# Optimization experiments

Hardware: AMD Instinct MI355X
Metric: run time of the kernel (lower is better)

The kernel has to match this reference:

```python
import jax, jax.numpy as jnp
import numpy as np

D = 2  # spatial dimension


def _conv_contract(image, filt, in_k, out_k):
    """Tensor convolution + contraction on a torus.
    image: (in_c, N, N) + (D,)*in_k
    filt:  (out_c, in_c, M, M) + (D,)*in_k + (D,)*out_k
    out:   (out_c, N, N) + (D,)*out_k
    Image tensor indices contract with the first in_k filter tensor indices.
    """
    in_c, N = image.shape[0], image.shape[1]
    out_c, M = filt.shape[0], filt.shape[2]
    di, do = D ** in_k, D ** out_k
    # fold tensor indices into channels: (1, in_c*di, N, N)
    img = jnp.transpose(image.reshape(in_c, N, N, di), (0, 3, 1, 2)).reshape(1, in_c * di, N, N)
    # filter -> (out_c*do, in_c*di, M, M), ordering (out_c, out_idx, in_c, in_idx)
    f = filt.reshape(out_c, in_c, M, M, di, do)
    f = jnp.transpose(f, (0, 5, 1, 4, 2, 3)).reshape(out_c * do, in_c * di, M, M)
    p = M // 2
    img = jnp.pad(img, ((0, 0), (0, 0), (p, p), (p, p)), mode='wrap')  # torus
    out = jax.lax.conv_general_dilated(
        img, f, window_strides=(1, 1), padding='VALID',
        dimension_numbers=('NCHW', 'OIHW', 'NCHW'))[0]
    out = jnp.transpose(out.reshape(out_c, do, N, N), (0, 2, 3, 1))
    return out.reshape((out_c, N, N) + (D,) * out_k)


def _synth(w, fils):
    # (out_c, in_c, n) x (n, M, M, tensor...) -> (out_c, in_c, M, M, tensor...)
    return jnp.einsum('oik,k...->oi...', w, fils)


def setup_inputs() -> dict:
    key = jax.random.key(0)
    ks = jax.random.split(key, 11)
    r = lambda k, s: jax.random.normal(k, s, dtype=jnp.float32)
    return {
        'x0': r(ks[0], (64, 256, 256)),
        'x1': r(ks[1], (64, 256, 256, 2)),
        'fil0': r(ks[2], (3, 3, 3)),
        'fil1': r(ks[3], (6, 3, 3, 2)),
        'fil2': r(ks[4], (12, 3, 3, 2, 2)),
        'w00': r(ks[5], (64, 64, 3)) * (1.0 / np.sqrt(64 * 3)),
        'w01': r(ks[6], (64, 64, 6)) * (1.0 / np.sqrt(64 * 6)),
        'w10': r(ks[7], (64, 64, 6)) * (1.0 / np.sqrt(64 * 6)),
        'w11': r(ks[8], (64, 64, 12)) * (1.0 / np.sqrt(64 * 12)),
        'b0': r(ks[9], (64, 1, 1)) * 0.05,
        'b1': r(ks[10], (64, 1, 1, 1)) * 0.05,
    }


def reference(x0, x1, fil0, fil1, fil2, w00, w01, w10, w11, b0, b1):
    # accumulate over input blocks for each target (out_k, out_p=0)
    out0 = _conv_contract(x0, _synth(w00, fil0), 0, 0) \
         + _conv_contract(x1, _synth(w10, fil1), 1, 0)
    out1 = _conv_contract(x0, _synth(w01, fil1), 0, 1) \
         + _conv_contract(x1, _synth(w11, fil2), 1, 1)
    # use_bias='auto': plain bias for scalars, mean-scaled bias for tensors
    out0 = out0 + b0
    mean1 = jnp.mean(out1, axis=(1, 2), keepdims=True)  # spatial mean
    out1 = out1 + mean1 * b1
    return (out0, out1)
```

## Files before the change

kernel.cpp:

```cpp
#include <hip/hip_runtime.h>
#include <hip/hip_bf16.h>
#include <string.h>


#define NN 256
#define NPIX 65536
#define OUT1_OFF 4194304

typedef __attribute__((ext_vector_type(8))) short short8;
typedef __attribute__((ext_vector_type(4))) float floatx4;

__device__ __forceinline__ unsigned short f2b(float x) {
    unsigned int u; memcpy(&u, &x, 4);
    return (unsigned short)((u + 0x7FFFu + ((u >> 16) & 1u)) >> 16);
}

__global__ __launch_bounds__(256) void prep_kernel(const float* __restrict__ x0,
                                                   const float* __restrict__ x1,
                                                   unsigned short* __restrict__ Xb) {
    const int x = threadIdx.x;
    const int y = blockIdx.x;
    const int c = blockIdx.y;
    unsigned int u[8];
    if (c < 4) {
        const float* base = x0 + ((size_t)c * 16) * NPIX + y * NN + x;
#pragma unroll
        for (int j = 0; j < 8; j++) {
            unsigned short a = f2b(base[(size_t)(2 * j) * NPIX]);
            unsigned short b = f2b(base[(size_t)(2 * j + 1) * NPIX]);
            u[j] = (unsigned int)a | ((unsigned int)b << 16);
        }
    } else {
        const float2* base = (const float2*)x1 + ((size_t)(8 * (c - 4))) * NPIX + y * NN + x;
#pragma unroll
        for (int j = 0; j < 8; j++) {
            float2 v = base[(size_t)j * NPIX];
            u[j] = (unsigned int)f2b(v.x) | ((unsigned int)f2b(v.y) << 16);
        }
    }
    uint4* dst = (uint4*)(Xb + (((size_t)y * 12 + c) * 256 + x) * 16);
    dst[0] = make_uint4(u[0], u[1], u[2], u[3]);
    dst[1] = make_uint4(u[4], u[5], u[6], u[7]);
}

__global__ void synth_kernel(const float* __restrict__ fil0, const float* __restrict__ fil1,
                             const float* __restrict__ fil2,
                             const float* __restrict__ w00, const float* __restrict__ w01,
                             const float* __restrict__ w10, const float* __restrict__ w11,
                             unsigned short* __restrict__ Fb) {
    int idx = blockIdx.x * 256 + threadIdx.x;
    if (idx >= 12 * 192 * 160) return;
    int kpos = idx % 160;
    int co   = (idx / 160) % 192;
    int c    = idx / (160 * 192);
    int tap = kpos >> 4, cl = kpos & 15;
    float s = 0.0f;
    if (tap < 9) {
        int cin = c * 16 + cl;
        if (co < 64) {
            if (cin < 64) {
                for (int k = 0; k < 3; k++)
                    s += w00[(co * 64 + cin) * 3 + k] * fil0[k * 9 + tap];
            } else {
                int i = (cin - 64) >> 1, t = (cin - 64) & 1;
                for (int k = 0; k < 6; k++)
                    s += w10[(co * 64 + i) * 6 + k] * fil1[(k * 9 + tap) * 2 + t];
            }
        } else {
            int o = (co - 64) >> 1, u = (co - 64) & 1;
            if (cin < 64) {
                for (int k = 0; k < 6; k++)
                    s += w01[(o * 64 + cin) * 6 + k] * fil1[(k * 9 + tap) * 2 + u];
            } else {
                int i = (cin - 64) >> 1, t = (cin - 64) & 1;
                for (int k = 0; k < 12; k++)
                    s += w11[(o * 64 + i) * 12 + k] * fil2[((k * 9 + tap) * 2 + t) * 2 + u];
            }
        }
    }
    Fb[idx] = f2b(s);
}

__global__ __launch_bounds__(512, 4) void conv_kernel(
    const unsigned short* __restrict__ Xb, const unsigned short* __restrict__ Fb,
    const float* __restrict__ b0, float* __restrict__ out,
    float* __restrict__ mean_partial) {

    __shared__ __align__(16) unsigned short Flds[96 * 160];
    __shared__ __align__(16) unsigned short Xlds[3 * 256 * 16];
    __shared__ float red[96][4];

    const int tid = threadIdx.x;
    const int y = blockIdx.x;
    const int m0 = blockIdx.y * 96;
    const int l = tid & 63, w = tid >> 6;
    const int wm = w >> 2, wn = w & 3;
    const int mw = wm * 48, nw = wn * 64;
    const int ln = l & 15, quad = l >> 4;

    int baseA[3];
#pragma unroll
    for (int f = 0; f < 3; f++) baseA[f] = (mw + f * 16 + ln) * 160 + quad * 8;
    int cb[4];
#pragma unroll
    for (int g = 0; g < 4; g++) cb[g] = nw + g * 16 + ln;
    int rofs[5], dxv[5];
#pragma unroll
    for (int ks = 0; ks < 5; ks++) {
        int tap = 2 * ks + (quad >> 1);
        int r, dx;
        if (tap > 8) { r = 0; dx = 0; }
        else { r = tap / 3; dx = tap - 3 * r - 1; }
        rofs[ks] = r * 4096 + (quad & 1) * 8;
        dxv[ks] = dx;
    }

    floatx4 acc[3][4];
#pragma unroll
    for (int f = 0; f < 3; f++)
#pragma unroll
        for (int g = 0; g < 4; g++) acc[f][g] = (floatx4){0.f, 0.f, 0.f, 0.f};

    for (int c = 0; c < 12; c++) {
        const unsigned short* FbC = Fb + ((size_t)c * 192 + m0) * 160;
        for (int s = w; s < 54; s += 8) {
            const unsigned short* g;
            unsigned short* lb;
            if (s < 30) {
                g = FbC + s * 512;
                lb = Flds + s * 512;
            } else {
                int j = s - 30;
                int r = j >> 3, p = j & 7;
                int yr = (y + r + 255) & 255;
                g = Xb + (((size_t)yr * 12 + c) * 4096) + p * 512;
                lb = Xlds + r * 4096 + p * 512;
            }
            __builtin_amdgcn_global_load_lds(
                (const __attribute__((address_space(1))) unsigned int*)(g + l * 8),
                (__attribute__((address_space(3))) unsigned int*)lb, 16, 0, 0);
        }
        __syncthreads();

#pragma unroll
        for (int ks = 0; ks < 5; ks++) {
            short8 A[3], B[4];
#pragma unroll
            for (int f = 0; f < 3; f++)
                A[f] = *(const short8*)(Flds + baseA[f] + ks * 32);
#pragma unroll
            for (int g = 0; g < 4; g++) {
                int colw = (cb[g] + dxv[ks]) & 255;
                B[g] = *(const short8*)(Xlds + rofs[ks] + colw * 16);
            }
#pragma unroll
            for (int f = 0; f < 3; f++)
#pragma unroll
                for (int g = 0; g < 4; g++)
                    acc[f][g] = __builtin_amdgcn_mfma_f32_16x16x32_bf16(A[f], B[g], acc[f][g], 0, 0, 0);
        }
        __syncthreads();
    }

#pragma unroll
    for (int f = 0; f < 3; f++)
#pragma unroll
        for (int reg = 0; reg < 4; reg++) {
            float s = acc[f][0][reg] + acc[f][1][reg] + acc[f][2][reg] + acc[f][3][reg];
#pragma unroll
            for (int d = 1; d < 16; d <<= 1) s += __shfl_xor(s, d, 64);
            if (ln == 0) red[mw + f * 16 + quad * 4 + reg][wn] = s;
        }

#pragma unroll
    for (int f = 0; f < 3; f++) {
        int cob = m0 + mw + f * 16 + quad * 4;
#pragma unroll
        for (int g = 0; g < 4; g++) {
            int col = nw + g * 16 + ln;
            if (cob < 64) {
#pragma unroll
                for (int reg = 0; reg < 4; reg++)
                    out[(size_t)(cob + reg) * NPIX + y * NN + col] = acc[f][g][reg] + b0[cob + reg];
            } else {
#pragma unroll
                for (int reg = 0; reg < 4; reg += 2) {
                    int o = (cob + reg - 64) >> 1;
                    float2 v = make_float2(acc[f][g][reg], acc[f][g][reg + 1]);
                    *((float2*)(out + OUT1_OFF) + ((size_t)o * NPIX + y * NN + col)) = v;
                }
            }
        }
    }
    __syncthreads();
    if (tid < 96) {
        int co = m0 + tid;
        if (co >= 64) {
            float s = red[tid][0] + red[tid][1] + red[tid][2] + red[tid][3];
            mean_partial[y * 128 + (co - 64)] = s;
        }
    }
}

__global__ void reduce_kernel(const float* __restrict__ mean_partial,
                              const float* __restrict__ b1, float* __restrict__ meanb) {
    int o = blockIdx.x;
    int t = threadIdx.x;
    float s0 = mean_partial[t * 128 + 2 * o];
    float s1 = mean_partial[t * 128 + 2 * o + 1];
#pragma unroll
    for (int d = 1; d < 64; d <<= 1) {
        s0 += __shfl_xor(s0, d, 64);
        s1 += __shfl_xor(s1, d, 64);
    }
    __shared__ float sh[2][4];
    if ((t & 63) == 0) { sh[0][t >> 6] = s0; sh[1][t >> 6] = s1; }
    __syncthreads();
    if (t == 0) {
        float S0 = sh[0][0] + sh[0][1] + sh[0][2] + sh[0][3];
        float S1 = sh[1][0] + sh[1][1] + sh[1][2] + sh[1][3];
        float scale = b1[o] * (1.0f / 65536.0f);
        meanb[2 * o] = S0 * scale;
        meanb[2 * o + 1] = S1 * scale;
    }
}

__global__ void apply_kernel(float* __restrict__ out, const float* __restrict__ meanb) {
    int idx = blockIdx.x * 256 + threadIdx.x;
    int o = idx >> 16;
    float2* p = (float2*)(out + OUT1_OFF) + idx;
    float2 v = *p;
    v.x += meanb[2 * o];
    v.y += meanb[2 * o + 1];
    *p = v;
}

extern "C" void kernel_launch(void* const* d_in, const int* in_sizes, int n_in,
                              void* d_out, int out_size, void* d_ws, size_t ws_size,
                              hipStream_t stream) {
    const float* x0   = (const float*)d_in[0];
    const float* x1   = (const float*)d_in[1];
    const float* fil0 = (const float*)d_in[2];
    const float* fil1 = (const float*)d_in[3];
    const float* fil2 = (const float*)d_in[4];
    const float* w00  = (const float*)d_in[5];
    const float* w01  = (const float*)d_in[6];
    const float* w10  = (const float*)d_in[7];
    const float* w11  = (const float*)d_in[8];
    const float* b0   = (const float*)d_in[9];
    const float* b1   = (const float*)d_in[10];

    unsigned short* Xb  = (unsigned short*)d_ws;
    unsigned short* Fb  = (unsigned short*)((char*)d_ws + 25165824);
    float* mean_partial = (float*)((char*)d_ws + 25903104);
    float* meanb        = (float*)((char*)d_ws + 26034176);
    float* out = (float*)d_out;

    prep_kernel<<<dim3(NN, 12), 256, 0, stream>>>(x0, x1, Xb);

    synth_kernel<<<(12 * 192 * 160 + 255) / 256, 256, 0, stream>>>(
        fil0, fil1, fil2, w00, w01, w10, w11, Fb);

    conv_kernel<<<dim3(NN, 2), 512, 0, stream>>>(Xb, Fb, b0, out, mean_partial);

    reduce_kernel<<<64, 256, 0, stream>>>(mean_partial, b1, meanb);

    apply_kernel<<<NPIX * 64 / 256, 256, 0, stream>>>(out, meanb);
}
```

Before: 175.1 us.

## Compute tensor-output spatial mean from input means and fold into conv epilogue

Uses linearity of the torus convolution to get the spatial mean of out1 from per-channel input means and the filter taps. Input sums are gathered during the bf16 prep pass, which now reads vectorised float4s. This removes the separate reduce and apply passes that re-read and re-wrote the whole out1 tensor, and lets conv add the mean bias directly when it stores. The filter row stride is padded to 168, and the mean is now taken over bf16-rounded filters against fp32 inputs, which slightly changes numerics.

```diff
diff --git a/kernel.cpp b/kernel.cpp
--- a/kernel.cpp
+++ b/kernel.cpp
@@ -6,6 +6,7 @@
 #define NN 256
 #define NPIX 65536
 #define OUT1_OFF 4194304
+#define FS 168
 
 typedef __attribute__((ext_vector_type(8))) short short8;
 typedef __attribute__((ext_vector_type(4))) float floatx4;
@@ -14,33 +15,63 @@
     unsigned int u; memcpy(&u, &x, 4);
     return (unsigned short)((u + 0x7FFFu + ((u >> 16) & 1u)) >> 16);
 }
+__device__ __forceinline__ float b2f16(unsigned short u) {
+    unsigned int v = ((unsigned int)u) << 16; float f; memcpy(&f, &v, 4); return f;
+}
+__device__ __forceinline__ unsigned int pack2(float a, float b) {
+    return (unsigned int)f2b(a) | ((unsigned int)f2b(b) << 16);
+}
 
 __global__ __launch_bounds__(256) void prep_kernel(const float* __restrict__ x0,
                                                    const float* __restrict__ x1,
-                                                   unsigned short* __restrict__ Xb) {
-    const int x = threadIdx.x;
-    const int y = blockIdx.x;
+                                                   unsigned short* __restrict__ Xb,
+                                                   float* __restrict__ partial) {
+    const int t = threadIdx.x;
+    const int w = t >> 6, tx = t & 63;
+    const int y = blockIdx.x * 4 + w;
     const int c = blockIdx.y;
-    unsigned int u[8];
+    const int col0 = tx * 4;
+
+    unsigned int u[4][8];
+    float sum[16];
     if (c < 4) {
-        const float* base = x0 + ((size_t)c * 16) * NPIX + y * NN + x;
-#pragma unroll
+        #pragma unroll
         for (int j = 0; j < 8; j++) {
-            unsigned short a = f2b(base[(size_t)(2 * j) * NPIX]);
-            unsigned short b = f2b(base[(size_t)(2 * j + 1) * NPIX]);
-            u[j] = (unsigned int)a | ((unsigned int)b << 16);
+            const float4 a = *(const float4*)(x0 + (size_t)(16 * c + 2 * j) * NPIX + y * NN + col0);
+            const float4 b = *(const float4*)(x0 + (size_t)(16 * c + 2 * j + 1) * NPIX + y * NN + col0);
+            u[0][j] = pack2(a.x, b.x);
+            u[1][j] = pack2(a.y, b.y);
+            u[2][j] = pack2(a.z, b.z);
+            u[3][j] = pack2(a.w, b.w);
+            sum[2 * j]     = a.x + a.y + a.z + a.w;
+            sum[2 * j + 1] = b.x + b.y + b.z + b.w;
         }
     } else {
-        const float2* base = (const float2*)x1 + ((size_t)(8 * (c - 4))) * NPIX + y * NN + x;
-#pragma unroll
+        #pragma unroll
         for (int j = 0; j < 8; j++) {
-            float2 v = base[(size_t)j * NPIX];
-            u[j] = (unsigned int)f2b(v.x) | ((unsigned int)f2b(v.y) << 16);
-        }
-    }
-    uint4* dst = (uint4*)(Xb + (((size_t)y * 12 + c) * 256 + x) * 16);
-    dst[0] = make_uint4(u[0], u[1], u[2], u[3]);
-    dst[1] = make_uint4(u[4], u[5], u[6], u[7]);
+            int i = 8 * (c - 4) + j;
+            const float* base = x1 + ((size_t)(i * 256 + y) * 256 + col0) * 2;
+            const float4 p0 = *(const float4*)(base);
+            const float4 p1 = *(const float4*)(base + 4);
+            u[0][j] = pack2(p0.x, p0.y);
+            u[1][j] = pack2(p0.z, p0.w);
+            u[2][j] = pack2(p1.x, p1.y);
+            u[3][j] = pack2(p1.z, p1.w);
+            sum[2 * j]     = p0.x + p0.z + p1.x + p1.z;
+            sum[2 * j + 1] = p0.y + p0.w + p1.y + p1.w;
+        }
+    }
+    uint4* dst = (uint4*)(Xb + (((size_t)y * 12 + c) * 256 + col0) * 16);
+    #pragma unroll
+    for (int cc = 0; cc < 4; cc++) {
+        dst[cc * 2]     = make_uint4(u[cc][0], u[cc][1], u[cc][2], u[cc][3]);
+        dst[cc * 2 + 1] = make_uint4(u[cc][4], u[cc][5], u[cc][6], u[cc][7]);
+    }
+    #pragma unroll
+    for (int cl = 0; cl < 16; cl++)
+        #pragma unroll
+        for (int d = 1; d < 64; d <<= 1) sum[cl] += __shfl_xor(sum[cl], d, 64);
+    if (tx < 16) partial[(c * 16 + tx) * 256 + y] = sum[tx];
 }
 
 __global__ void synth_kernel(const float* __restrict__ fil0, const float* __restrict__ fil1,
@@ -49,10 +80,10 @@
                              const float* __restrict__ w10, const float* __restrict__ w11,
                              unsigned short* __restrict__ Fb) {
     int idx = blockIdx.x * 256 + threadIdx.x;
-    if (idx >= 12 * 192 * 160) return;
-    int kpos = idx % 160;
-    int co   = (idx / 160) % 192;
-    int c    = idx / (160 * 192);
+    if (idx >= 12 * 192 * FS) return;
+    int kpos = idx % FS;
+    int co   = (idx / FS) % 192;
+    int c    = idx / (FS * 192);
     int tap = kpos >> 4, cl = kpos & 15;
     float s = 0.0f;
     if (tap < 9) {
@@ -81,14 +112,40 @@
     Fb[idx] = f2b(s);
 }
 
+__global__ void meanx_kernel(const float* __restrict__ partial, float* __restrict__ meanX) {
+    int cin = blockIdx.x * 64 + threadIdx.x;
+    const float4* p = (const float4*)(partial + (size_t)cin * 256);
+    float s = 0.0f;
+    for (int j = 0; j < 64; j++) { float4 v = p[j]; s += v.x + v.y + v.z + v.w; }
+    meanX[cin] = s * (1.0f / 65536.0f);
+}
+
+__global__ void meanb_kernel(const unsigned short* __restrict__ Fb,
+                             const float* __restrict__ meanX,
+                             const float* __restrict__ b1, float* __restrict__ meanb) {
+    int c1 = blockIdx.x;
+    int l = threadIdx.x;
+    int co = 64 + c1;
+    float s = 0.0f;
+    for (int c = 0; c < 12; c++) {
+        const unsigned short* row = Fb + ((size_t)c * 192 + co) * FS;
+        for (int idx = l; idx < 144; idx += 64) {
+            int tap = idx >> 4, cl = idx & 15;
+            s += b2f16(row[tap * 16 + cl]) * meanX[c * 16 + cl];
+        }
+    }
+    #pragma unroll
+    for (int d = 1; d < 64; d <<= 1) s += __shfl_xor(s, d, 64);
+    if (l == 0) meanb[c1] = s * b1[c1 >> 1];
+}
+
 __global__ __launch_bounds__(512, 4) void conv_kernel(
     const unsigned short* __restrict__ Xb, const unsigned short* __restrict__ Fb,
-    const float* __restrict__ b0, float* __restrict__ out,
-    float* __restrict__ mean_partial) {
-
-    __shared__ __align__(16) unsigned short Flds[96 * 160];
+    const float* __restrict__ b0, const float* __restrict__ meanb,
+    float* __restrict__ out) {
+
+    __shared__ __align__(16) unsigned short Flds[16384];
     __shared__ __align__(16) unsigned short Xlds[3 * 256 * 16];
-    __shared__ float red[96][4];
 
     const int tid = threadIdx.x;
     const int y = blockIdx.x;
@@ -100,7 +157,7 @@
 
     int baseA[3];
 #pragma unroll
-    for (int f = 0; f < 3; f++) baseA[f] = (mw + f * 16 + ln) * 160 + quad * 8;
+    for (int f = 0; f < 3; f++) baseA[f] = (mw + f * 16 + ln) * FS + quad * 8;
     int cb[4];
 #pragma unroll
     for (int g = 0; g < 4; g++) cb[g] = nw + g * 16 + ln;
@@ -122,15 +179,15 @@
         for (int g = 0; g < 4; g++) acc[f][g] = (floatx4){0.f, 0.f, 0.f, 0.f};
 
     for (int c = 0; c < 12; c++) {
-        const unsigned short* FbC = Fb + ((size_t)c * 192 + m0) * 160;
-        for (int s = w; s < 54; s += 8) {
+        const unsigned short* FbC = Fb + ((size_t)c * 192 + m0) * FS;
+        for (int s = w; s < 56; s += 8) {
             const unsigned short* g;
             unsigned short* lb;
-            if (s < 30) {
+            if (s < 32) {
                 g = FbC + s * 512;
                 lb = Flds + s * 512;
             } else {
-                int j = s - 30;
+                int j = s - 32;
                 int r = j >> 3, p = j & 7;
                 int yr = (y + r + 255) & 255;
                 g = Xb + (((size_t)yr * 12 + c) * 4096) + p * 512;
@@ -163,16 +220,6 @@
     }
 
 #pragma unroll
-    for (int f = 0; f < 3; f++)
-#pragma unroll
-        for (int reg = 0; reg < 4; reg++) {
-            float s = acc[f][0][reg] + acc[f][1][reg] + acc[f][2][reg] + acc[f][3][reg];
-#pragma unroll
-            for (int d = 1; d < 16; d <<= 1) s += __shfl_xor(s, d, 64);
-            if (ln == 0) red[mw + f * 16 + quad * 4 + reg][wn] = s;
-        }
-
-#pragma unroll
     for (int f = 0; f < 3; f++) {
         int cob = m0 + mw + f * 16 + quad * 4;
 #pragma unroll
@@ -185,54 +232,15 @@
             } else {
 #pragma unroll
                 for (int reg = 0; reg < 4; reg += 2) {
-                    int o = (cob + reg - 64) >> 1;
-                    float2 v = make_float2(acc[f][g][reg], acc[f][g][reg + 1]);
+                    int c1 = cob + reg - 64;
+                    int o = c1 >> 1;
+                    float2 v = make_float2(acc[f][g][reg] + meanb[c1],
+                                           acc[f][g][reg + 1] + meanb[c1 + 1]);
                     *((float2*)(out + OUT1_OFF) + ((size_t)o * NPIX + y * NN + col)) = v;
                 }
             }
         }
     }
-    __syncthreads();
-    if (tid < 96) {
-        int co = m0 + tid;
-        if (co >= 64) {
-            float s = red[tid][0] + red[tid][1] + red[tid][2] + red[tid][3];
-            mean_partial[y * 128 + (co - 64)] = s;
-        }
-    }
-}
-
-__global__ void reduce_kernel(const float* __restrict__ mean_partial,
-                              const float* __restrict__ b1, float* __restrict__ meanb) {
-    int o = blockIdx.x;
-    int t = threadIdx.x;
-    float s0 = mean_partial[t * 128 + 2 * o];
-    float s1 = mean_partial[t * 128 + 2 * o + 1];
-#pragma unroll
-    for (int d = 1; d < 64; d <<= 1) {
-        s0 += __shfl_xor(s0, d, 64);
-        s1 += __shfl_xor(s1, d, 64);
-    }
-    __shared__ float sh[2][4];
-    if ((t & 63) == 0) { sh[0][t >> 6] = s0; sh[1][t >> 6] = s1; }
-    __syncthreads();
-    if (t == 0) {
-        float S0 = sh[0][0] + sh[0][1] + sh[0][2] + sh[0][3];
-        float S1 = sh[1][0] + sh[1][1] + sh[1][2] + sh[1][3];
-        float scale = b1[o] * (1.0f / 65536.0f);
-        meanb[2 * o] = S0 * scale;
-        meanb[2 * o + 1] = S1 * scale;
-    }
-}
-
-__global__ void apply_kernel(float* __restrict__ out, const float* __restrict__ meanb) {
-    int idx = blockIdx.x * 256 + threadIdx.x;
-    int o = idx >> 16;
-    float2* p = (float2*)(out + OUT1_OFF) + idx;
-    float2 v = *p;
-    v.x += meanb[2 * o];
-    v.y += meanb[2 * o + 1];
-    *p = v;
 }
 
 extern "C" void kernel_launch(void* const* d_in, const int* in_sizes, int n_in,
@@ -250,20 +258,21 @@
     const float* b0   = (const float*)d_in[9];
     const float* b1   = (const float*)d_in[10];
 
-    unsigned short* Xb  = (unsigned short*)d_ws;
-    unsigned short* Fb  = (unsigned short*)((char*)d_ws + 25165824);
-    float* mean_partial = (float*)((char*)d_ws + 25903104);
-    float* meanb        = (float*)((char*)d_ws + 26034176);
+    unsigned short* Xb = (unsigned short*)d_ws;
+    unsigned short* Fb = (unsigned short*)((char*)d_ws + 25165824);
+    float* partial     = (float*)((char*)d_ws + 25940480);
+    float* meanX       = (float*)((char*)d_ws + 26137088);
+    float* meanb       = (float*)((char*)d_ws + 26138112);
     float* out = (float*)d_out;
 
-    prep_kernel<<<dim3(NN, 12), 256, 0, stream>>>(x0, x1, Xb);
-
-    synth_kernel<<<(12 * 192 * 160 + 255) / 256, 256, 0, stream>>>(
+    prep_kernel<<<dim3(64, 12), 256, 0, stream>>>(x0, x1, Xb, partial);
+
+    synth_kernel<<<(12 * 192 * FS + 255) / 256, 256, 0, stream>>>(
         fil0, fil1, fil2, w00, w01, w10, w11, Fb);
 
-    conv_kernel<<<dim3(NN, 2), 512, 0, stream>>>(Xb, Fb, b0, out, mean_partial);
-
-    reduce_kernel<<<64, 256, 0, stream>>>(mean_partial, b1, meanb);
-
-    apply_kernel<<<NPIX * 64 / 256, 256, 0, stream>>>(out, meanb);
-}
+    meanx_kernel<<<3, 64, 0, stream>>>(partial, meanX);
+
+    meanb_kernel<<<128, 64, 0, stream>>>(Fb, meanX, b1, meanb);
+
+    conv_kernel<<<dim3(NN, 2), 512, 0, stream>>>(Xb, Fb, b0, meanb, out);
+}
```

Result: slower. 178.9 us (+2.2%).
